# Optimization experiments

Measured on AMD Instinct MI355X. Metric: run time of the kernel, lower is better.

Reference implementation:

```python
import jax, jax.numpy as jnp
import numpy as np

T, B, D, NH, DH, MEM = 1024, 4, 1024, 8, 128, 1024
LIM = 1024  # PositionalEmbedding lim default


def setup_inputs() -> dict:
    key = jax.random.key(0)
    ks = jax.random.split(key, 11)
    h = jax.random.normal(ks[0], (T, B, D), jnp.float32)
    m = jax.random.normal(ks[1], (MEM, B, D), jnp.float32)
    q_w = jax.random.normal(ks[2], (NH * DH, D), jnp.float32) * 0.02
    k_w = jax.random.normal(ks[3], (NH * DH, D), jnp.float32) * 0.02
    r_w = jax.random.normal(ks[4], (NH * DH, D), jnp.float32) * 0.02
    k_bias = jax.random.normal(ks[5], (NH, DH), jnp.float32)  # torch init normal(0,1)
    r_bias = jax.random.normal(ks[6], (NH, DH), jnp.float32)
    ln_scale = jnp.ones((D,), jnp.float32)
    ln_bias = jnp.zeros((D,), jnp.float32)
    reset = jax.random.uniform(ks[7], (T, B)) < 0.01       # sparse episode resets
    old_reset = jax.random.uniform(ks[8], (MEM, B)) < 0.01
    return dict(h=h, m=m, q_w=q_w, k_w=k_w, r_w=r_w, k_bias=k_bias, r_bias=r_bias,
                ln_scale=ln_scale, ln_bias=ln_bias, reset=reset, old_reset=old_reset)


def layer_norm(x, scale, bias, eps=1e-5):
    mu = jnp.mean(x, axis=-1, keepdims=True)
    var = jnp.mean(jnp.square(x - mu), axis=-1, keepdims=True)
    return (x - mu) * jax.lax.rsqrt(var + eps) * scale + bias


def rel_shift(x):
    # x: [T, C, B, N] -> Transformer-XL relative shift
    t, c = x.shape[:2]
    tail = x.shape[2:]
    zero_pad = jnp.zeros((t, 1) + tail, x.dtype)
    x_padded = jnp.concatenate([zero_pad, x], axis=1).reshape((c + 1, t) + tail)
    return x_padded[1:].reshape(x.shape)


def reference(h, m, q_w, k_w, r_w, k_bias, r_bias, ln_scale, ln_bias, reset, old_reset):
    t, b = h.shape[:2]
    mm = m.shape[0]
    tm = t + mm
    # ---- ResetMasker: cols[i,b,j] = any reset at i' with j < i' <= i ----
    resets = jnp.concatenate([old_reset, reset], 0).astype(jnp.int32)  # [L, B]
    cum = jnp.cumsum(resets, axis=0)                                   # [L, B]
    reset_mask = (cum[-t:, None, :] - cum[None, :, :]) > 0             # [T, L, B]
    reset_mask = reset_mask[:, -tm:]                                   # [T, TM, B]
    # ---- default attention mask ----
    i = jnp.arange(t)[:, None]
    j = jnp.arange(tm)[None, :]
    mask_len = mm + t - MEM
    mask_shift_len = (t - mask_len) if mask_len > 0 else t
    future_mask = j >= i + mm          # triu(ones, M + future=0)
    history_mask = j <= i - mask_shift_len
    default_mask = (future_mask | history_mask)[:, :, None]            # [T, TM, 1]
    mask = (reset_mask | default_mask)[:, :, :, None]                  # [T, TM, B, 1]
    # ---- projections ----
    cat = layer_norm(jnp.concatenate([m, h], axis=0), ln_scale, ln_bias)  # [TM, B, D]
    q = (cat[-t:] @ q_w.T).reshape(t, b, NH, DH)
    k = (cat @ k_w.T).reshape(tm, b, NH, DH)
    score = jnp.einsum('ibnd,jbnd->ijbn', q + k_bias, k)               # [T, TM, B, NH]
    # ---- relative position term ----
    pos_seq = jnp.arange(tm - 1, -1, -1, dtype=h.dtype)
    inv_freq = 2.0 * jnp.pi / LIM ** (jnp.arange(0, D, 2, dtype=jnp.float32) / D)
    sinusoid = pos_seq[:, None] * inv_freq                              # [TM, D/2]
    pe = jnp.concatenate([jnp.sin(sinusoid), jnp.cos(sinusoid)], -1)    # [TM, D]
    r = (pe @ r_w.T).reshape(tm, NH, DH)
    pos_score = jnp.einsum('ibnd,jnd->ijbn', q + r_bias, r)             # [T, TM, B, NH]
    score = score + rel_shift(pos_score)
    # ---- scale, mask, clamp, softmax ----
    score = jnp.where(mask, -65000.0, score / np.sqrt(DH))
    score = jnp.clip(score, -65000.0, 65000.0)
    prob = jax.nn.softmax(score, axis=1)
    all_masked = jnp.all(mask, axis=1, keepdims=True)                   # [T, 1, B, 1]
    return jnp.where(all_masked, 0.0, prob)
```

## Files before the change

kernel.cpp:

```cpp
#include <hip/hip_runtime.h>
#include <hip/hip_bf16.h>
#include <stdint.h>

typedef __bf16 bf16;
typedef __bf16 bf16x4 __attribute__((ext_vector_type(4)));
typedef __bf16 bf16x8 __attribute__((ext_vector_type(8)));
typedef float f32x4 __attribute__((ext_vector_type(4)));

__device__ __forceinline__ void gload_lds16(const void* g, void* l) {
  __builtin_amdgcn_global_load_lds((const __attribute__((address_space(1))) void*)g,
                                   (__attribute__((address_space(3))) void*)l, 16, 0, 0);
}

#define WAITV(N) asm volatile("s_waitcnt vmcnt(" #N ")" ::: "memory")
__device__ __forceinline__ void barx() {
  __builtin_amdgcn_sched_barrier(0);
  __builtin_amdgcn_s_barrier();
  __builtin_amdgcn_sched_barrier(0);
}

__global__ void setup_kernel(const void* __restrict__ rst, const void* __restrict__ orst,
                             int* __restrict__ jmin) {
  __shared__ int sflag;
  int tid = threadIdx.x;
  if (tid == 0) sflag = 0;
  __syncthreads();
  int local = 0;
  for (int idx = tid; idx < 1024; idx += 256) {
    unsigned v1 = ((const unsigned*)rst)[idx];
    unsigned v2 = ((const unsigned*)orst)[idx];
    unsigned vv[2] = {v1, v2};
    for (int t = 0; t < 2; ++t) {
      unsigned v = vv[t];
      if (v == 0x3F800000u) local |= 1;
      else if (v > 1u) local |= 2;
    }
  }
  if (local) atomicOr(&sflag, local);
  __syncthreads();
  int mode = (sflag & 2) ? 2 : ((sflag & 1) ? 1 : 0);
  int lane = tid & 63, w = tid >> 6;
  if (w < 4) {
    int b = w;
    int rv[32];
    int lmax = -1;
#pragma unroll
    for (int u = 0; u < 32; ++u) {
      int s = lane * 32 + u;
      int idx = (s < 1024) ? s * 4 + b : (s - 1024) * 4 + b;
      const void* p = (s < 1024) ? orst : rst;
      int x;
      if (mode == 2)      x = ((const unsigned char*)p)[idx] != 0;
      else if (mode == 1) x = ((const float*)p)[idx] != 0.0f;
      else                x = ((const int*)p)[idx] != 0;
      rv[u] = x;
      if (x) lmax = s;
    }
    int inc = lmax;
    for (int o = 1; o < 64; o <<= 1) {
      int oth = __shfl_up(inc, o);
      if (lane >= o && oth > inc) inc = oth;
    }
    int cur = __shfl_up(inc, 1);
    if (lane == 0) cur = -1;
#pragma unroll
    for (int u = 0; u < 32; ++u) {
      int s = lane * 32 + u;
      if (rv[u]) cur = s;
      if (s >= 1024) jmin[(s - 1024) * 4 + b] = (cur > 0) ? cur : 0;
    }
  }
}

__global__ __launch_bounds__(256) void ln_kernel(const float* __restrict__ h, const float* __restrict__ mm,
                                                 const float* __restrict__ sc, const float* __restrict__ bi,
                                                 bf16* __restrict__ catln) {
  int row = blockIdx.x;
  const float* src = (row < 4096) ? (mm + (size_t)row * 1024) : (h + (size_t)(row - 4096) * 1024);
  int tid = threadIdx.x;
  float4 v = ((const float4*)src)[tid];
  float s1 = v.x + v.y + v.z + v.w;
  float s2 = v.x * v.x + v.y * v.y + v.z * v.z + v.w * v.w;
  int lane = tid & 63, w = tid >> 6;
  for (int o = 32; o; o >>= 1) { s1 += __shfl_down(s1, o); s2 += __shfl_down(s2, o); }
  __shared__ float red[8];
  if (lane == 0) { red[w] = s1; red[w + 4] = s2; }
  __syncthreads();
  float S1 = red[0] + red[1] + red[2] + red[3];
  float S2 = red[4] + red[5] + red[6] + red[7];
  float mean = S1 * (1.0f / 1024.0f);
  float var = S2 * (1.0f / 1024.0f) - mean * mean;
  float rstd = rsqrtf(var + 1e-5f);
  bf16x4 o;
#pragma unroll
  for (int c = 0; c < 4; ++c) {
    float x = (c == 0) ? v.x : (c == 1) ? v.y : (c == 2) ? v.z : v.w;
    o[c] = (bf16)((x - mean) * rstd * sc[tid * 4 + c] + bi[tid * 4 + c]);
  }
  *(bf16x4*)(catln + (size_t)row * 1024 + tid * 4) = o;
}

__global__ __launch_bounds__(256) void prep_kernel(const float* __restrict__ qw, const float* __restrict__ kw,
                                                   const float* __restrict__ rw, bf16* __restrict__ qwb,
                                                   bf16* __restrict__ kwb, bf16* __restrict__ rwb,
                                                   bf16* __restrict__ pe) {
  size_t id = (size_t)blockIdx.x * 256 + threadIdx.x;
  if (id < 3145728) {
    const float* s = id < 1048576 ? qw : (id < 2097152 ? kw : rw);
    bf16* d = id < 1048576 ? qwb : (id < 2097152 ? kwb : rwb);
    size_t o = id & 1048575;
    d[o] = (bf16)s[o];
  } else {
    size_t p = id - 3145728;
    int jj = (int)(p >> 10), dcol = (int)(p & 1023);
    float pos = (float)(2047 - jj);
    int fi = dcol < 512 ? dcol : dcol - 512;
    float f = exp2f(-0.01953125f * (float)fi);
    float rev = pos * f;
    rev -= floorf(rev);
    float ang = 6.283185307179586f * rev;
    pe[p] = (bf16)(dcol < 512 ? __sinf(ang) : __cosf(ang));
  }
}

__device__ __forceinline__ size_t out_index(int mode, int row, int col) {
  int n = col >> 7, dh = col & 127;
  if (mode <= 0) { int i = row >> 2, b = row & 3; return ((size_t)(b * 8 + n) * 1024 + i) * 128 + dh; }
  if (mode == 1) { int s = row >> 2, b = row & 3; return ((size_t)(b * 8 + n) * 2048 + s) * 128 + dh; }
  return ((size_t)n * 2048 + row) * 128 + dh;
}

__global__ __launch_bounds__(256) void gemm_all(const bf16* __restrict__ catln, const bf16* __restrict__ pe,
                                                const bf16* __restrict__ qwb, const bf16* __restrict__ kwb,
                                                const bf16* __restrict__ rwb, const float* __restrict__ kbias,
                                                const float* __restrict__ rbias, bf16* __restrict__ qkb,
                                                bf16* __restrict__ qrb, bf16* __restrict__ kkv,
                                                bf16* __restrict__ rrv) {
  __shared__ alignas(16) char lA[8192];
  __shared__ alignas(16) char lB[8192];
  const int K = 1024;
  int by = blockIdx.y;
  const bf16* A; const bf16* W; int mode; int brow;
  if (by < 32)      { mode = 0; A = catln + (size_t)4096 * 1024; W = qwb; brow = by << 7; }
  else if (by < 96) { mode = 1; A = catln;                        W = kwb; brow = (by - 32) << 7; }
  else              { mode = 2; A = pe;                           W = rwb; brow = (by - 96) << 7; }
  int tid = threadIdx.x;
  int lane = tid & 63, w = tid >> 6;
  int bcol = blockIdx.x << 7;
  int wr = w >> 1, wc = w & 1;
  f32x4 acc[4][4] = {};
  int r0 = tid >> 2;
  int c8 = (tid & 3) << 3;
  const bf16* gA0 = A + (size_t)(brow + r0) * K + c8;
  const bf16* gB0 = W + (size_t)(bcol + r0) * K + c8;
  char* lAw = lA + w * 1024;
  char* lBw = lB + w * 1024;
  for (int k0 = 0; k0 < K; k0 += 32) {
    if (k0) __syncthreads();
    gload_lds16(gA0 + k0, lAw);
    gload_lds16(gA0 + (size_t)64 * K + k0, lAw + 4096);
    gload_lds16(gB0 + k0, lBw);
    gload_lds16(gB0 + (size_t)64 * K + k0, lBw + 4096);
    __syncthreads();
    const char* pa = lA + (((wr << 6) + (lane & 15)) << 6) + ((lane >> 4) << 4);
    const char* pb = lB + (((wc << 6) + (lane & 15)) << 6) + ((lane >> 4) << 4);
    bf16x8 af[4], bfr[4];
#pragma unroll
    for (int x = 0; x < 4; ++x) {
      af[x] = *(const bf16x8*)(pa + (x << 10));
      bfr[x] = *(const bf16x8*)(pb + (x << 10));
    }
#pragma unroll
    for (int mi = 0; mi < 4; ++mi)
#pragma unroll
      for (int ni = 0; ni < 4; ++ni)
        acc[mi][ni] = __builtin_amdgcn_mfma_f32_16x16x32_bf16(af[mi], bfr[ni], acc[mi][ni], 0, 0, 0);
  }
  int rowb = brow + (wr << 6) + ((lane >> 4) << 2);
  int colb = bcol + (wc << 6) + (lane & 15);
#pragma unroll
  for (int mi = 0; mi < 4; ++mi)
#pragma unroll
    for (int ni = 0; ni < 4; ++ni) {
      int col = colb + (ni << 4);
      float bk = 0.0f, br = 0.0f;
      if (mode == 0) { bk = kbias[col]; br = rbias[col]; }
#pragma unroll
      for (int v = 0; v < 4; ++v) {
        int row = rowb + (mi << 4) + v;
        size_t idx = out_index(mode, row, col);
        if (mode == 0) {
          qkb[idx] = (bf16)(acc[mi][ni][v] + bk);
          qrb[idx] = (bf16)(acc[mi][ni][v] + br);
        } else if (mode == 1) {
          kkv[idx] = (bf16)acc[mi][ni][v];
        } else {
          rrv[idx] = (bf16)acc[mi][ni][v];
        }
      }
    }
}

__global__ __launch_bounds__(256, 2) void score2_kernel(const bf16* __restrict__ qk, const bf16* __restrict__ qr,
                                                        const bf16* __restrict__ kk, const bf16* __restrict__ rr,
                                                        const int* __restrict__ jmin, bf16* __restrict__ P,
                                                        float* __restrict__ scaleBuf) {
  __shared__ float sl[64 * 128];
  __shared__ alignas(16) bf16 stg[4][32 * 128];
  __shared__ int jl_s[64];
  int tid = threadIdx.x, lane = tid & 63;
  int w = (tid >> 6) & 3;
  int bid0 = blockIdx.x;
  int bid = ((bid0 & 7) << 6) | (bid0 >> 3);
  int bn = bid >> 4;
  int it = bid & 15;
  int i0 = it << 6;
  int b = bn >> 3, n = bn & 7;
  int r15 = lane & 15, kc = lane >> 4;
  int il0 = w << 4;
  int g4 = kc << 2;
  const float scale = 0.08838834764831845f;

  if (tid < 64) jl_s[tid] = jmin[(i0 + tid) * 4 + b];

  bf16x8 aK[4], aR[4];
  {
    const bf16* qkrow = qk + ((size_t)bn * 1024 + i0 + il0 + r15) * 128 + kc * 8;
    const bf16* qrrow = qr + ((size_t)bn * 1024 + i0 + il0 + r15) * 128 + kc * 8;
#pragma unroll
    for (int ks = 0; ks < 4; ++ks) {
      aK[ks] = *(const bf16x8*)(qkrow + ks * 32);
      aR[ks] = *(const bf16x8*)(qrrow + ks * 32);
    }
  }

  int su1 = tid, su2 = tid + 256;
  int srow1 = su1 >> 4, scol1 = (su1 & 15) ^ (srow1 & 7);
  int srow2 = su2 >> 4, scol2 = (su2 & 15) ^ (srow2 & 7);
  char* dst1 = (char*)stg + (size_t)(su1 & ~63) * 16;
  char* dst2 = (char*)stg + (size_t)(su2 & ~63) * 16;
  const bf16* rbase = rr + (size_t)n * 2048 * 128;
  const bf16* kbase = kk + (size_t)bn * 2048 * 128;

  auto issue_t = [&](int ci, int si, int buf) {
    const bf16* base = (si < 4) ? rbase : kbase;
    int row0 = (si < 4) ? (1023 + (ci << 7) + (si << 5)) : (i0 + (ci << 7) + ((si - 4) << 5));
    size_t bo = (size_t)buf * 8192;
    gload_lds16(base + (size_t)(row0 + srow1) * 128 + scol1 * 8, dst1 + bo);
    gload_lds16(base + (size_t)(row0 + srow2) * 128 + scol2 * 8, dst2 + bo);
  };

  int xsw = (((il0 >> 2) + kc) & 7) << 4;
  f32x4 s2r[8];

  issue_t(0, 0, 0); issue_t(0, 1, 1); issue_t(0, 2, 2);
  for (int c = 0; c < 8; ++c) {
    int c128 = c << 7;
#pragma unroll
    for (int s = 0; s < 10; ++s) {
      int t = c * 10 + s;
      if (s <= 6)      issue_t(c, s + 3, ((c << 1) + s + 3) & 3);
      else if (c < 7)  issue_t(c + 1, s - 7, ((c << 1) + s + 3) & 3);
      int rem = 79 - t;
      if (rem >= 3)      WAITV(6);
      else if (rem == 2) WAITV(4);
      else if (rem == 1) WAITV(2);
      else               WAITV(0);
      barx();
      const char* sb = (const char*)stg + (size_t)(((c << 1) + s) & 3) * 8192;
      if (s < 4) {
#pragma unroll
        for (int cf = 0; cf < 2; ++cf) {
          int fr = (cf << 4) + r15;
          f32x4 acc = {};
#pragma unroll
          for (int ks = 0; ks < 4; ++ks) {
            int lcol = (ks << 2) + kc;
            bf16x8 bf = *(const bf16x8*)(sb + fr * 256 + ((lcol ^ (fr & 7)) << 4));
            acc = __builtin_amdgcn_mfma_f32_16x16x32_bf16(aR[ks], bf, acc, 0, 0, 0);
          }
          s2r[s * 2 + cf] = acc;
        }
      } else {
        int s1 = s - 4;
#pragma unroll
        for (int cf = 0; cf < 2; ++cf) {
          int jl0 = (s1 << 5) + (cf << 4);
          int doff = jl0 - il0;
          if (doff < -15 || doff > 142) continue;
          int fr = (cf << 4) + r15;
          f32x4 acc = {};
#pragma unroll
          for (int ks = 0; ks < 4; ++ks) {
            int lcol = (ks << 2) + kc;
            bf16x8 bf = *(const bf16x8*)(sb + fr * 256 + ((lcol ^ (fr & 7)) << 4));
            acc = __builtin_amdgcn_mfma_f32_16x16x32_bf16(aK[ks], bf, acc, 0, 0, 0);
          }
          int dbase = jl0 + r15 - il0 - g4;
#pragma unroll
          for (int v = 0; v < 4; ++v) {
            int ddl = dbase - v;
            if ((unsigned)ddl < 128u) {
              sl[(il0 + g4 + v) * 128 + (ddl ^ xsw)] = acc[v];
            }
          }
        }
      }
      if (s == 9) {
#pragma unroll
        for (int v = 0; v < 4; ++v) {
          int il = il0 + g4 + v;
          int ig = i0 + il;
          int jm = jl_s[il];
          int lo = (ig + 1 > jm) ? ig + 1 : jm;
          int ddlo = lo - ig;
          float vals[8];
          float mx = -3.0e38f;
#pragma unroll
          for (int u = 0; u < 8; ++u) {
            int ddc = (u << 4) + r15;
            float x = (s2r[u][v] + sl[il * 128 + (ddc ^ xsw)]) * scale;
            x = fminf(fmaxf(x, -65000.0f), 65000.0f);
            float xm = ((c128 + ddc) >= ddlo) ? x : -3.0e38f;
            vals[u] = xm;
            mx = fmaxf(mx, xm);
          }
          for (int o = 8; o; o >>= 1) mx = fmaxf(mx, __shfl_xor(mx, o));
          float sum = 0.0f;
#pragma unroll
          for (int u = 0; u < 8; ++u) {
            float e = (vals[u] > -1.0e38f) ? __expf(vals[u] - mx) : 0.0f;
            vals[u] = e;
            sum += e;
          }
          for (int o = 8; o; o >>= 1) sum += __shfl_xor(sum, o);
          size_t pbase = ((size_t)bn * 1024 + ig) * 1024;
#pragma unroll
          for (int u = 0; u < 8; ++u) {
            int dd = c128 + (u << 4) + r15;
            P[pbase + (((dd >> 3) ^ (bn & 7)) << 3) + (dd & 7)] = (bf16)vals[u];
          }
          if (r15 == 0) {
            float2 ms = make_float2(mx, sum);
            *(float2*)(scaleBuf + (((size_t)ig * 32 + bn) * 8 + c) * 2) = ms;
          }
        }
      }
      barx();
    }
  }
}

__global__ __launch_bounds__(256) void score_full(const bf16* __restrict__ qk, const bf16* __restrict__ qr,
                                                  const bf16* __restrict__ kk, const bf16* __restrict__ rr,
                                                  const int* __restrict__ jmin, float* __restrict__ out) {
  __shared__ float sl[16 * 1024];
  int tid = threadIdx.x, lane = tid & 63, w = tid >> 6;
  int bid = blockIdx.x;
  int i0 = (bid & 63) << 4;
  int bn = bid >> 6;
  int b = bn >> 3, n = bn & 7;
  int r15 = lane & 15, kc = lane >> 4;
  bf16x8 aq[4], ar[4];
  {
    const bf16* qkrow = qk + ((size_t)bn * 1024 + i0 + r15) * 128 + kc * 8;
    const bf16* qrrow = qr + ((size_t)bn * 1024 + i0 + r15) * 128 + kc * 8;
#pragma unroll
    for (int f = 0; f < 4; ++f) {
      aq[f] = *(const bf16x8*)(qkrow + f * 32);
      ar[f] = *(const bf16x8*)(qrrow + f * 32);
    }
  }
  for (int t = w; t < 64; t += 4) {
    int dd0 = t << 4;
    const bf16* rrow = rr + ((size_t)n * 2048 + 1023 + dd0 + r15) * 128 + kc * 8;
    f32x4 acc = {};
#pragma unroll
    for (int f = 0; f < 4; ++f)
      acc = __builtin_amdgcn_mfma_f32_16x16x32_bf16(ar[f], *(const bf16x8*)(rrow + f * 32), acc, 0, 0, 0);
    int dd = dd0 + r15;
#pragma unroll
    for (int v = 0; v < 4; ++v) sl[(kc * 4 + v) * 1024 + dd] = acc[v];
  }
  __syncthreads();
  for (int t = w; t < 65; t += 4) {
    int j0 = i0 + (t << 4);
    const bf16* krow = kk + ((size_t)bn * 2048 + j0 + r15) * 128 + kc * 8;
    f32x4 acc = {};
#pragma unroll
    for (int f = 0; f < 4; ++f)
      acc = __builtin_amdgcn_mfma_f32_16x16x32_bf16(aq[f], *(const bf16x8*)(krow + f * 32), acc, 0, 0, 0);
    int jc = (t << 4) + r15;
#pragma unroll
    for (int v = 0; v < 4; ++v) {
      int ii = kc * 4 + v;
      int dd = jc - ii;
      if (dd >= 1 && dd <= 1023) sl[ii * 1024 + dd] += acc[v];
    }
  }
  __syncthreads();
  const float scale = 0.08838834764831845f;
  for (int ii = w; ii < 16; ii += 4) {
    int i = i0 + ii;
    int jm = jmin[i * 4 + b];
    int lo = (i + 1 > jm) ? i + 1 : jm;
    int ddlo = lo - i;
    size_t ob = (size_t)i * 65536 + bn;
    if (ddlo > 1023) {
      for (int j = lane; j < 2048; j += 64) out[ob + (size_t)j * 32] = 0.0f;
      continue;
    }
    float vals[16];
    float mx = -3.0e38f;
#pragma unroll
    for (int c = 0; c < 16; ++c) {
      int dd = (c << 6) + lane;
      float x = sl[ii * 1024 + dd] * scale;
      x = fminf(fmaxf(x, -65000.0f), 65000.0f);
      float xm = (dd >= ddlo) ? x : -3.0e38f;
      vals[c] = xm;
      mx = fmaxf(mx, xm);
    }
    for (int o = 32; o; o >>= 1) mx = fmaxf(mx, __shfl_xor(mx, o));
    float sum = 0.0f;
#pragma unroll
    for (int c = 0; c < 16; ++c) {
      float e = (vals[c] > -1.0e38f) ? __expf(vals[c] - mx) : 0.0f;
      vals[c] = e;
      sum += e;
    }
    for (int o = 32; o; o >>= 1) sum += __shfl_xor(sum, o);
    float inv = 1.0f / sum;
    for (int j = lane; j < 2048; j += 64) {
      int dd = j - i;
      float pv = 0.0f;
      if (dd >= ddlo && dd <= 1023) {
        float x = sl[ii * 1024 + dd] * scale;
        x = fminf(fmaxf(x, -65000.0f), 65000.0f);
        pv = __expf(x - mx) * inv;
      }
      out[ob + (size_t)j * 32] = pv;
    }
  }
}

__global__ __launch_bounds__(256) void scatter_kernel(const bf16* __restrict__ P,
                                                      const float* __restrict__ scaleBuf,
                                                      float* __restrict__ out) {
  __shared__ alignas(16) bf16 ld[32 * 1024];
  __shared__ float sc_l[32 * 8];
  int i = blockIdx.x;
  int tid = threadIdx.x;
#pragma unroll
  for (int it = 0; it < 16; ++it) {
    int c = it * 256 + tid;
    int bn = c >> 7, u = c & 127;
    const bf16* src = P + ((size_t)bn * 1024 + i) * 1024 + u * 8;
    gload_lds16(src, (char*)ld + (size_t)(it * 256 + (tid & ~63)) * 16);
  }
  {
    int bn_t = tid >> 3, c_t = tid & 7;
    const float2* sp = (const float2*)(scaleBuf + ((size_t)i * 32 + bn_t) * 16);
    float m[8], s[8];
#pragma unroll
    for (int k = 0; k < 8; ++k) { float2 p = sp[k]; m[k] = p.x; s[k] = p.y; }
    float M = m[0];
#pragma unroll
    for (int k = 1; k < 8; ++k) M = fmaxf(M, m[k]);
    float S = 0.0f;
#pragma unroll
    for (int k = 0; k < 8; ++k) S += s[k] * __expf(m[k] - M);
    sc_l[bn_t * 8 + c_t] = (S > 0.0f) ? (__expf(m[c_t] - M) / S) : 0.0f;
  }
  __syncthreads();
  int bn0 = (tid & 7) << 2;
  int jb = tid >> 3;
  size_t ob = (size_t)i * 65536;
  for (int it = 0; it < 64; ++it) {
    int j = it * 32 + jb;
    int dd = j - i;
    f32x4 v = {0.0f, 0.0f, 0.0f, 0.0f};
    if (dd >= 1 && dd <= 1023) {
      int u = dd >> 3, lo = (dd & 7) << 1, cc = dd >> 7;
#pragma unroll
      for (int e = 0; e < 4; ++e) {
        int bn = bn0 + e;
        const bf16* p = (const bf16*)((const char*)ld + bn * 2048 + (((u ^ (bn & 7)) << 4) | lo));
        v[e] = (float)*p * sc_l[bn * 8 + cc];
      }
    }
    *(f32x4*)(out + ob + (size_t)j * 32 + bn0) = v;
  }
}

extern "C" void kernel_launch(void* const* d_in, const int* in_sizes, int n_in,
                              void* d_out, int out_size, void* d_ws, size_t ws_size,
                              hipStream_t stream) {
  const float* h   = (const float*)d_in[0];
  const float* m   = (const float*)d_in[1];
  const float* qw  = (const float*)d_in[2];
  const float* kw  = (const float*)d_in[3];
  const float* rw  = (const float*)d_in[4];
  const float* kb  = (const float*)d_in[5];
  const float* rb  = (const float*)d_in[6];
  const float* lns = (const float*)d_in[7];
  const float* lnb = (const float*)d_in[8];
  const void*  rst = d_in[9];
  const void* orst = d_in[10];
  float* out = (float*)d_out;
  char* ws = (char*)d_ws;

  int* jmin   = (int*)ws;
  bf16* catln = (bf16*)(ws + 65536);
  bf16* qwb   = catln + (size_t)8192 * 1024;
  bf16* kwb   = qwb + (size_t)1024 * 1024;
  bf16* rwb   = kwb + (size_t)1024 * 1024;
  bf16* pe    = rwb + (size_t)1024 * 1024;
  bf16* qkb   = pe + (size_t)2048 * 1024;
  bf16* qrb   = qkb + (size_t)4096 * 1024;
  bf16* kk    = qrb + (size_t)4096 * 1024;
  bf16* rr    = kk + (size_t)8192 * 1024;
  bf16* P     = rr + (size_t)2048 * 1024;
  float* scaleBuf = (float*)(P + (size_t)33554432);
  size_t need_fast = (size_t)((char*)(scaleBuf + 524288) - ws);
  bool fast = ws_size >= need_fast;

  setup_kernel<<<1, 256, 0, stream>>>(rst, orst, jmin);
  ln_kernel<<<8192, 256, 0, stream>>>(h, m, lns, lnb, catln);
  prep_kernel<<<20480, 256, 0, stream>>>(qw, kw, rw, qwb, kwb, rwb, pe);
  gemm_all<<<dim3(8, 112), 256, 0, stream>>>(catln, pe, qwb, kwb, rwb, kb, rb, qkb, qrb, kk, rr);
  if (fast) {
    score2_kernel<<<512, 256, 0, stream>>>(qkb, qrb, kk, rr, jmin, P, scaleBuf);
    scatter_kernel<<<1024, 256, 0, stream>>>(P, scaleBuf, out);
  } else {
    score_full<<<2048, 256, 0, stream>>>(qkb, qrb, kk, rr, jmin, out);
  }
}
```

Before: 222.0 us.

## Restructure score2 staging into double-buffered 64-row tile pairs with one barrier

```diff
diff --git a/kernel.cpp b/kernel.cpp
--- a/kernel.cpp
+++ b/kernel.cpp
@@ -10,13 +10,6 @@
 __device__ __forceinline__ void gload_lds16(const void* g, void* l) {
   __builtin_amdgcn_global_load_lds((const __attribute__((address_space(1))) void*)g,
                                    (__attribute__((address_space(3))) void*)l, 16, 0, 0);
-}
-
-#define WAITV(N) asm volatile("s_waitcnt vmcnt(" #N ")" ::: "memory")
-__device__ __forceinline__ void barx() {
-  __builtin_amdgcn_sched_barrier(0);
-  __builtin_amdgcn_s_barrier();
-  __builtin_amdgcn_sched_barrier(0);
 }
 
 __global__ void setup_kernel(const void* __restrict__ rst, const void* __restrict__ orst,
@@ -206,7 +199,7 @@
                                                         const int* __restrict__ jmin, bf16* __restrict__ P,
                                                         float* __restrict__ scaleBuf) {
   __shared__ float sl[64 * 128];
-  __shared__ alignas(16) bf16 stg[4][32 * 128];
+  __shared__ alignas(16) bf16 stg[2][64 * 128];
   __shared__ int jl_s[64];
   int tid = threadIdx.x, lane = tid & 63;
   int w = (tid >> 6) & 3;
@@ -237,41 +230,45 @@
   int su1 = tid, su2 = tid + 256;
   int srow1 = su1 >> 4, scol1 = (su1 & 15) ^ (srow1 & 7);
   int srow2 = su2 >> 4, scol2 = (su2 & 15) ^ (srow2 & 7);
-  char* dst1 = (char*)stg + (size_t)(su1 & ~63) * 16;
-  char* dst2 = (char*)stg + (size_t)(su2 & ~63) * 16;
+  size_t do1 = (size_t)(su1 & ~63) * 16;
+  size_t do2 = (size_t)(su2 & ~63) * 16;
   const bf16* rbase = rr + (size_t)n * 2048 * 128;
   const bf16* kbase = kk + (size_t)bn * 2048 * 128;
 
-  auto issue_t = [&](int ci, int si, int buf) {
-    const bf16* base = (si < 4) ? rbase : kbase;
-    int row0 = (si < 4) ? (1023 + (ci << 7) + (si << 5)) : (i0 + (ci << 7) + ((si - 4) << 5));
-    size_t bo = (size_t)buf * 8192;
-    gload_lds16(base + (size_t)(row0 + srow1) * 128 + scol1 * 8, dst1 + bo);
-    gload_lds16(base + (size_t)(row0 + srow2) * 128 + scol2 * 8, dst2 + bo);
+  auto issue_pair = [&](int pg) {
+    if (pg >= 40) return;
+    char* bufb = (char*)stg + (size_t)(pg & 1) * 16384;
+#pragma unroll
+    for (int k = 0; k < 2; ++k) {
+      int ti = pg * 2 + k;
+      int ci = ti / 10, si = ti - ci * 10;
+      const bf16* base = (si < 4) ? rbase : kbase;
+      int row0 = (si < 4) ? (1023 + (ci << 7) + (si << 5)) : (i0 + (ci << 7) + ((si - 4) << 5));
+      char* db = bufb + (size_t)k * 8192;
+      gload_lds16(base + (size_t)(row0 + srow1) * 128 + scol1 * 8, db + do1);
+      gload_lds16(base + (size_t)(row0 + srow2) * 128 + scol2 * 8, db + do2);
+    }
   };
 
   int xsw = (((il0 >> 2) + kc) & 7) << 4;
+  int pu0 = (((lane >> 3) ^ (bn & 7)) << 3) | (lane & 7);
   f32x4 s2r[8];
 
-  issue_t(0, 0, 0); issue_t(0, 1, 1); issue_t(0, 2, 2);
+  issue_pair(0);
   for (int c = 0; c < 8; ++c) {
     int c128 = c << 7;
 #pragma unroll
-    for (int s = 0; s < 10; ++s) {
-      int t = c * 10 + s;
-      if (s <= 6)      issue_t(c, s + 3, ((c << 1) + s + 3) & 3);
-      else if (c < 7)  issue_t(c + 1, s - 7, ((c << 1) + s + 3) & 3);
-      int rem = 79 - t;
-      if (rem >= 3)      WAITV(6);
-      else if (rem == 2) WAITV(4);
-      else if (rem == 1) WAITV(2);
-      else               WAITV(0);
-      barx();
-      const char* sb = (const char*)stg + (size_t)(((c << 1) + s) & 3) * 8192;
-      if (s < 4) {
-#pragma unroll
-        for (int cf = 0; cf < 2; ++cf) {
-          int fr = (cf << 4) + r15;
+    for (int q = 0; q < 5; ++q) {
+      int g = c * 5 + q;
+      __syncthreads();
+      issue_pair(g + 1);
+      const char* pb = (const char*)stg + (size_t)(g & 1) * 16384;
+      __builtin_amdgcn_s_setprio(1);
+      if (q < 2) {
+#pragma unroll
+        for (int sc = 0; sc < 4; ++sc) {
+          const char* sb = pb + (sc >> 1) * 8192;
+          int fr = ((sc & 1) << 4) + r15;
           f32x4 acc = {};
 #pragma unroll
           for (int ks = 0; ks < 4; ++ks) {
@@ -279,16 +276,16 @@
             bf16x8 bf = *(const bf16x8*)(sb + fr * 256 + ((lcol ^ (fr & 7)) << 4));
             acc = __builtin_amdgcn_mfma_f32_16x16x32_bf16(aR[ks], bf, acc, 0, 0, 0);
           }
-          s2r[s * 2 + cf] = acc;
+          s2r[q * 4 + sc] = acc;
         }
       } else {
-        int s1 = s - 4;
-#pragma unroll
-        for (int cf = 0; cf < 2; ++cf) {
-          int jl0 = (s1 << 5) + (cf << 4);
+#pragma unroll
+        for (int sc = 0; sc < 4; ++sc) {
+          int jl0 = ((q - 2) << 6) + (sc << 4);
           int doff = jl0 - il0;
           if (doff < -15 || doff > 142) continue;
-          int fr = (cf << 4) + r15;
+          const char* sb = pb + (sc >> 1) * 8192;
+          int fr = ((sc & 1) << 4) + r15;
           f32x4 acc = {};
 #pragma unroll
           for (int ks = 0; ks < 4; ++ks) {
@@ -306,7 +303,8 @@
           }
         }
       }
-      if (s == 9) {
+      __builtin_amdgcn_s_setprio(0);
+      if (q == 4) {
 #pragma unroll
         for (int v = 0; v < 4; ++v) {
           int il = il0 + g4 + v;
@@ -346,7 +344,6 @@
           }
         }
       }
-      barx();
     }
   }
 }
```

After: 217.1 us. 1.02x faster.

## Switch score2 staging to a double buffer and raise occupancy to three blocks

Applied to the files above, without the earlier changes.

```diff
diff --git a/kernel.cpp b/kernel.cpp
--- a/kernel.cpp
+++ b/kernel.cpp
@@ -10,13 +10,6 @@
 __device__ __forceinline__ void gload_lds16(const void* g, void* l) {
   __builtin_amdgcn_global_load_lds((const __attribute__((address_space(1))) void*)g,
                                    (__attribute__((address_space(3))) void*)l, 16, 0, 0);
-}
-
-#define WAITV(N) asm volatile("s_waitcnt vmcnt(" #N ")" ::: "memory")
-__device__ __forceinline__ void barx() {
-  __builtin_amdgcn_sched_barrier(0);
-  __builtin_amdgcn_s_barrier();
-  __builtin_amdgcn_sched_barrier(0);
 }
 
 __global__ void setup_kernel(const void* __restrict__ rst, const void* __restrict__ orst,
@@ -201,12 +194,12 @@
     }
 }
 
-__global__ __launch_bounds__(256, 2) void score2_kernel(const bf16* __restrict__ qk, const bf16* __restrict__ qr,
+__global__ __launch_bounds__(256, 3) void score2_kernel(const bf16* __restrict__ qk, const bf16* __restrict__ qr,
                                                         const bf16* __restrict__ kk, const bf16* __restrict__ rr,
                                                         const int* __restrict__ jmin, bf16* __restrict__ P,
                                                         float* __restrict__ scaleBuf) {
   __shared__ float sl[64 * 128];
-  __shared__ alignas(16) bf16 stg[4][32 * 128];
+  __shared__ alignas(16) bf16 stg[2][32 * 128];
   __shared__ int jl_s[64];
   int tid = threadIdx.x, lane = tid & 63;
   int w = (tid >> 6) & 3;
@@ -237,37 +230,32 @@
   int su1 = tid, su2 = tid + 256;
   int srow1 = su1 >> 4, scol1 = (su1 & 15) ^ (srow1 & 7);
   int srow2 = su2 >> 4, scol2 = (su2 & 15) ^ (srow2 & 7);
-  char* dst1 = (char*)stg + (size_t)(su1 & ~63) * 16;
-  char* dst2 = (char*)stg + (size_t)(su2 & ~63) * 16;
+  size_t do1 = (size_t)(su1 & ~63) * 16;
+  size_t do2 = (size_t)(su2 & ~63) * 16;
   const bf16* rbase = rr + (size_t)n * 2048 * 128;
   const bf16* kbase = kk + (size_t)bn * 2048 * 128;
 
   auto issue_t = [&](int ci, int si, int buf) {
     const bf16* base = (si < 4) ? rbase : kbase;
     int row0 = (si < 4) ? (1023 + (ci << 7) + (si << 5)) : (i0 + (ci << 7) + ((si - 4) << 5));
-    size_t bo = (size_t)buf * 8192;
-    gload_lds16(base + (size_t)(row0 + srow1) * 128 + scol1 * 8, dst1 + bo);
-    gload_lds16(base + (size_t)(row0 + srow2) * 128 + scol2 * 8, dst2 + bo);
+    char* db = (char*)stg + (size_t)buf * 8192;
+    gload_lds16(base + (size_t)(row0 + srow1) * 128 + scol1 * 8, db + do1);
+    gload_lds16(base + (size_t)(row0 + srow2) * 128 + scol2 * 8, db + do2);
   };
 
   int xsw = (((il0 >> 2) + kc) & 7) << 4;
   f32x4 s2r[8];
 
-  issue_t(0, 0, 0); issue_t(0, 1, 1); issue_t(0, 2, 2);
+  issue_t(0, 0, 0);
   for (int c = 0; c < 8; ++c) {
     int c128 = c << 7;
 #pragma unroll
     for (int s = 0; s < 10; ++s) {
-      int t = c * 10 + s;
-      if (s <= 6)      issue_t(c, s + 3, ((c << 1) + s + 3) & 3);
-      else if (c < 7)  issue_t(c + 1, s - 7, ((c << 1) + s + 3) & 3);
-      int rem = 79 - t;
-      if (rem >= 3)      WAITV(6);
-      else if (rem == 2) WAITV(4);
-      else if (rem == 1) WAITV(2);
-      else               WAITV(0);
-      barx();
-      const char* sb = (const char*)stg + (size_t)(((c << 1) + s) & 3) * 8192;
+      __syncthreads();
+      if (s < 9)      issue_t(c, s + 1, (s + 1) & 1);
+      else if (c < 7) issue_t(c + 1, 0, 0);
+      const char* sb = (const char*)stg + (size_t)(s & 1) * 8192;
+      __builtin_amdgcn_s_setprio(1);
       if (s < 4) {
 #pragma unroll
         for (int cf = 0; cf < 2; ++cf) {
@@ -282,10 +270,9 @@
           s2r[s * 2 + cf] = acc;
         }
       } else {
-        int s1 = s - 4;
 #pragma unroll
         for (int cf = 0; cf < 2; ++cf) {
-          int jl0 = (s1 << 5) + (cf << 4);
+          int jl0 = ((s - 4) << 5) + (cf << 4);
           int doff = jl0 - il0;
           if (doff < -15 || doff > 142) continue;
           int fr = (cf << 4) + r15;
@@ -306,6 +293,7 @@
           }
         }
       }
+      __builtin_amdgcn_s_setprio(0);
       if (s == 9) {
 #pragma unroll
         for (int v = 0; v < 4; ++v) {
@@ -346,7 +334,6 @@
           }
         }
       }
-      barx();
     }
   }
 }
```

Result: slower. 328.4 us (+48.0%).
